# Optimization experiments

Hardware: AMD Instinct MI355X
Metric: run time of the kernel (lower is better)

## Reference

```python
import jax, jax.numpy as jnp
import numpy as np

B, S, D, H = 2, 2048, 768, 12
DK = D // H

def setup_inputs() -> dict:
    key = jax.random.key(0)
    ks = jax.random.split(key, 5)
    scale = 1.0 / np.sqrt(D)
    return {
        "X": jax.random.normal(ks[0], (B, S, D), dtype=jnp.float32),
        "Wq": jax.random.normal(ks[1], (D, D), dtype=jnp.float32) * scale,
        "Wk": jax.random.normal(ks[2], (D, D), dtype=jnp.float32) * scale,
        "Wv": jax.random.normal(ks[3], (D, D), dtype=jnp.float32) * scale,
        "Wo": jax.random.normal(ks[4], (D, D), dtype=jnp.float32) * scale,
    }

def reference(X, Wq, Wk, Wv, Wo):
    # torch Linear: y = x @ W.T  (no bias in this repo's Linear)
    Q = X @ Wq.T  # (B,S,D)
    K = X @ Wk.T
    V = X @ Wv.T
    def split_heads(t):
        return t.reshape(B, S, H, DK).transpose(0, 2, 1, 3)  # (B,H,S,DK)
    Qh, Kh, Vh = split_heads(Q), split_heads(K), split_heads(V)
    scores = jnp.einsum('bhqd,bhkd->bhqk', Qh, Kh) / jnp.sqrt(jnp.float32(DK))
    causal = jnp.tril(jnp.ones((S, S), dtype=bool))  # keep lower triangle
    scores = jnp.where(causal, scores, -jnp.inf)
    attn = jax.nn.softmax(scores, axis=-1)
    out_h = jnp.einsum('bhqk,bhkd->bhqd', attn, Vh)  # (B,H,S,DK)
    out = out_h.transpose(0, 2, 1, 3).reshape(B, S, D)
    return out @ Wo.T
```

## Files before the change

kernel.cpp:

```cpp
#include <hip/hip_runtime.h>
#include <stdint.h>

#define BB   2
#define SS   2048
#define DD   768
#define HH   12
#define MM   (BB*SS)
#define XSZ  (MM*DD)
#define WSZ  (DD*DD)

typedef __bf16 v8bf __attribute__((ext_vector_type(8)));
typedef float  v4f  __attribute__((ext_vector_type(4)));

__device__ inline v4f mfma16(v8bf a, v8bf b, v4f c) {
    return __builtin_amdgcn_mfma_f32_16x16x32_bf16(a, b, c, 0, 0, 0);
}

__device__ inline unsigned short f2bf(float f) {
    union { float f; uint32_t u; } v; v.f = f;
    return (unsigned short)((v.u + 0x7FFFu + ((v.u >> 16) & 1u)) >> 16);
}

__device__ inline uint4 cvt8(const float* __restrict__ p) {
    uint4 out;
    unsigned short* s = (unsigned short*)&out;
#pragma unroll
    for (int j = 0; j < 8; ++j) s[j] = f2bf(p[j]);
    return out;
}

__device__ __forceinline__ void gld_lds16(const unsigned short* g, unsigned short* l) {
    __builtin_amdgcn_global_load_lds(
        (const __attribute__((address_space(1))) void*)g,
        (__attribute__((address_space(3))) void*)l, 16, 0, 0);
}

__global__ __launch_bounds__(256) void cvt_w3(
    const float* __restrict__ Wq, const float* __restrict__ Wk,
    const float* __restrict__ Wv, unsigned short* __restrict__ dst)
{
    long i4 = ((long)blockIdx.x * 256 + threadIdx.x) * 4;
    int t = (int)(i4 / WSZ);
    long off = i4 - (long)t * WSZ;
    const float* s = (t == 0) ? Wq : (t == 1) ? Wk : Wv;
    float4 v = *(const float4*)(s + off);
    ushort4 o;
    o.x = f2bf(v.x); o.y = f2bf(v.y); o.z = f2bf(v.z); o.w = f2bf(v.w);
    *(ushort4*)(dst + (size_t)t * WSZ + off) = o;
}

template<int A_ASYNC, int W_ASYNC, int C_F32, int VT2>
__global__ __launch_bounds__(256) void gemm_64(
    const void* __restrict__ Ain,
    const void* __restrict__ W0, const void* __restrict__ W1,
    const void* __restrict__ W2,
    void* __restrict__ C0, void* __restrict__ C1, void* __restrict__ C2)
{
    const int K = DD, N = DD;
    const void* W = W0;
    void* C = C0;
    if (blockIdx.z == 1) { W = W1; C = C1; }
    else if (blockIdx.z == 2) { W = W2; C = C2; }

    __shared__ __align__(16) unsigned short As[64 * 32];
    __shared__ __align__(16) unsigned short Bs[64 * 32];

    const int tid  = threadIdx.x;
    const int wave = tid >> 6, lane = tid & 63;
    const int quad = lane >> 4, l16 = lane & 15;
    const int waveM = (wave >> 1) * 32, waveN = (wave & 1) * 32;
    const int m0 = blockIdx.y * 64, n0 = blockIdx.x * 64;

    const int rS = (tid >> 2), cS = (tid & 3) * 8;

    v4f acc[2][2] = {};

    for (int kt = 0; kt < K; kt += 32) {
        __syncthreads();
        if (A_ASYNC)
            gld_lds16((const unsigned short*)Ain + (size_t)(m0 + rS) * K + kt + cS,
                      &As[wave * 512]);
        else
            *(uint4*)(&As[tid * 8]) = cvt8((const float*)Ain + (size_t)(m0 + rS) * K + kt + cS);
        if (W_ASYNC)
            gld_lds16((const unsigned short*)W + (size_t)(n0 + rS) * K + kt + cS,
                      &Bs[wave * 512]);
        else
            *(uint4*)(&Bs[tid * 8]) = cvt8((const float*)W + (size_t)(n0 + rS) * K + kt + cS);
        __syncthreads();

        v8bf af[2], bf[2];
#pragma unroll
        for (int i = 0; i < 2; ++i) {
            af[i] = *(const v8bf*)(&As[(waveM + i * 16 + l16) * 32 + quad * 8]);
            bf[i] = *(const v8bf*)(&Bs[(waveN + i * 16 + l16) * 32 + quad * 8]);
        }
#pragma unroll
        for (int mi = 0; mi < 2; ++mi)
#pragma unroll
            for (int ni = 0; ni < 2; ++ni)
                acc[mi][ni] = mfma16(af[mi], bf[ni], acc[mi][ni]);
    }

#pragma unroll
    for (int mi = 0; mi < 2; ++mi)
#pragma unroll
        for (int ni = 0; ni < 2; ++ni)
#pragma unroll
            for (int r = 0; r < 4; ++r) {
                int row = m0 + waveM + mi * 16 + quad * 4 + r;
                int col = n0 + waveN + ni * 16 + l16;
                if (VT2 && blockIdx.z == 2) {
                    int b = row >> 11, s = row & 2047;
                    int h = col >> 6,  dk = col & 63;
                    ((unsigned short*)C)[(((size_t)(b * HH + h)) * 64 + dk) * SS + s] =
                        f2bf(acc[mi][ni][r]);
                } else if (C_F32) {
                    ((float*)C)[(size_t)row * N + col] = acc[mi][ni][r];
                } else {
                    ((unsigned short*)C)[(size_t)row * N + col] = f2bf(acc[mi][ni][r]);
                }
            }
}

__global__ __launch_bounds__(256, 3) void attn_ls(
    const unsigned short* Q,
    const unsigned short* __restrict__ Kg,
    const unsigned short* __restrict__ Vt,
    unsigned short* O)
{
    const int h = blockIdx.x, b = blockIdx.y;
    const int qs = (SS / 64 - 1 - (int)blockIdx.z) * 64;
    const int tid  = threadIdx.x;
    const int wave = tid >> 6, lane = tid & 63;
    const int quad = lane >> 4, l16 = lane & 15;
    const int qw = qs + wave * 16;
    const float scale = 0.125f;

    __shared__ __align__(16) unsigned short Ks[2][4096];
    __shared__ __align__(16) unsigned short Vs[2][4096];
    __shared__ __align__(16) unsigned short Ps[4][16 * 72];

    v8bf qf0, qf1;
    {
        const unsigned short* qp = &Q[((size_t)(b * SS + qw + l16)) * DD + h * 64];
        qf0 = *(const v8bf*)(qp + quad * 8);
        qf1 = *(const v8bf*)(qp + 32 + quad * 8);
    }

    const int NT = qs / 64 + 1;
    const char* kgb = (const char*)&Kg[(size_t)(b * SS) * DD + h * 64];
    const char* vgb = (const char*)&Vt[((size_t)(b * HH + h) * 64) * SS];

    const int rA = wave * 8 + (lane >> 3);
    const int oA = ((lane & 7) * 16) ^ ((rA & 7) << 4);
    const int swz = (l16 & 7) << 4;

    v4f oacc[4] = {};
    float l_run[4] = {0.f, 0.f, 0.f, 0.f};
    unsigned short* pw = &Ps[wave][0];

    gld_lds16((const unsigned short*)(kgb + (size_t)rA        * (DD * 2) + oA), &Ks[0][wave * 512]);
    gld_lds16((const unsigned short*)(kgb + (size_t)(rA + 32) * (DD * 2) + oA), &Ks[0][2048 + wave * 512]);
    gld_lds16((const unsigned short*)(vgb + (size_t)rA        * (SS * 2) + oA), &Vs[0][wave * 512]);
    gld_lds16((const unsigned short*)(vgb + (size_t)(rA + 32) * (SS * 2) + oA), &Vs[0][2048 + wave * 512]);
    __syncthreads();

    for (int kt = 0; kt < NT; ++kt) {
        const int cur = kt & 1;
        const int kb  = kt * 64;

        if (kt + 1 < NT) {
            const size_t kb2 = (size_t)(kb + 64);
            gld_lds16((const unsigned short*)(kgb + (kb2 + rA)      * (DD * 2) + oA), &Ks[cur ^ 1][wave * 512]);
            gld_lds16((const unsigned short*)(kgb + (kb2 + rA + 32) * (DD * 2) + oA), &Ks[cur ^ 1][2048 + wave * 512]);
            gld_lds16((const unsigned short*)(vgb + (size_t)rA        * (SS * 2) + kb2 * 2 + oA), &Vs[cur ^ 1][wave * 512]);
            gld_lds16((const unsigned short*)(vgb + (size_t)(rA + 32) * (SS * 2) + kb2 * 2 + oA), &Vs[cur ^ 1][2048 + wave * 512]);
        }

        const char* ksb = (const char*)&Ks[cur][0];
        const char* vsb = (const char*)&Vs[cur][0];

        v8bf kf0[4], kf1[4];
#pragma unroll
        for (int nk = 0; nk < 4; ++nk) {
            const char* krow = ksb + (size_t)(nk * 16 + l16) * 128;
            kf0[nk] = *(const v8bf*)(krow + ((quad * 16) ^ swz));
            kf1[nk] = *(const v8bf*)(krow + ((64 + quad * 16) ^ swz));
        }

        v4f sacc[4] = {};
#pragma unroll
        for (int nk = 0; nk < 4; ++nk) {
            sacc[nk] = mfma16(qf0, kf0[nk], sacc[nk]);
            sacc[nk] = mfma16(qf1, kf1[nk], sacc[nk]);
        }

        const bool diag = (kt == NT - 1);
        float pv[4][4];
#pragma unroll
        for (int nk = 0; nk < 4; ++nk)
#pragma unroll
            for (int r = 0; r < 4; ++r) {
                float p = __expf(sacc[nk][r] * scale);
                if (diag) {
                    int key  = kb + nk * 16 + l16;
                    int qrow = qw + quad * 4 + r;
                    if (key > qrow) p = 0.0f;
                }
                pv[nk][r] = p;
                l_run[r] += p;
            }

        v8bf vf[2][4];
#pragma unroll
        for (int kc = 0; kc < 2; ++kc)
#pragma unroll
            for (int dt = 0; dt < 4; ++dt) {
                const char* vr = vsb + (size_t)(dt * 16 + l16) * 128;
                vf[kc][dt] = *(const v8bf*)(vr + ((kc * 64 + quad * 16) ^ swz));
            }

#pragma unroll
        for (int nk = 0; nk < 4; ++nk)
#pragma unroll
            for (int r = 0; r < 4; ++r)
                pw[(quad * 4 + r) * 72 + nk * 16 + l16] = f2bf(pv[nk][r]);
        __asm__ volatile("" ::: "memory");

        v8bf pa0 = *(const v8bf*)(&pw[l16 * 72 + quad * 8]);
        v8bf pa1 = *(const v8bf*)(&pw[l16 * 72 + 32 + quad * 8]);
#pragma unroll
        for (int dt = 0; dt < 4; ++dt) oacc[dt] = mfma16(pa0, vf[0][dt], oacc[dt]);
#pragma unroll
        for (int dt = 0; dt < 4; ++dt) oacc[dt] = mfma16(pa1, vf[1][dt], oacc[dt]);

        __syncthreads();
    }

    for (int off = 1; off < 16; off <<= 1)
#pragma unroll
        for (int r = 0; r < 4; ++r)
            l_run[r] += __shfl_xor(l_run[r], off, 64);

    float inv[4];
#pragma unroll
    for (int r = 0; r < 4; ++r) inv[r] = 1.0f / l_run[r];

    unsigned short* ob = &O[((size_t)(b * SS + qw + quad * 4)) * DD + h * 64 + l16];
#pragma unroll
    for (int r = 0; r < 4; ++r)
#pragma unroll
        for (int dt = 0; dt < 4; ++dt)
            ob[(size_t)r * DD + dt * 16] = f2bf(oacc[dt][r] * inv[r]);
}

extern "C" void kernel_launch(void* const* d_in, const int* in_sizes, int n_in,
                              void* d_out, int out_size, void* d_ws, size_t ws_size,
                              hipStream_t stream)
{
    const float* X  = (const float*)d_in[0];
    const float* Wq = (const float*)d_in[1];
    const float* Wk = (const float*)d_in[2];
    const float* Wv = (const float*)d_in[3];
    const float* Wo = (const float*)d_in[4];
    float* Out = (float*)d_out;

    unsigned short* Qb  = (unsigned short*)d_ws;
    unsigned short* Kb  = Qb + XSZ;
    unsigned short* Vtb = (unsigned short*)d_out;
    unsigned short* Wqb = Vtb + XSZ;
    unsigned short* Wkb = Wqb + WSZ;
    unsigned short* Wvb = Wkb + WSZ;

    dim3 blk(256);
    cvt_w3<<<1728, blk, 0, stream>>>(Wq, Wk, Wv, Wqb);

    dim3 g1(DD / 64, MM / 64, 3);
    gemm_64<0, 1, 0, 1><<<g1, blk, 0, stream>>>(X, Wqb, Wkb, Wvb, Qb, Kb, Vtb);

    dim3 g2(HH, BB, SS / 64);
    attn_ls<<<g2, blk, 0, stream>>>(Qb, Kb, Vtb, Qb);

    dim3 g3(DD / 64, MM / 64, 1);
    gemm_64<1, 0, 1, 0><<<g3, blk, 0, stream>>>(Qb, Wo, Wo, Wo, Out, Out, Out);
}
```

Before: 183.3 us.

## Fuse QKV projections into one kernel sharing converted X tiles

Replaces the three-way z-indexed QKV GEMM with one kernel that converts each X tile to bf16 once and multiplies it against Wq, Wk and Wv tiles held together in LDS, using a 64-deep K step, XOR-swizzled shared layouts and a grouped block ordering. It also pre-converts Wo to bf16 into the free K buffer so the output GEMM can load weights asynchronously. The aim is to cut repeated X loads and fp32 conversions and to shrink weight traffic. In exchange it raises LDS use and accumulator register pressure, which may lower occupancy, and it adds an extra conversion launch.

```diff
diff --git a/kernel.cpp b/kernel.cpp
--- a/kernel.cpp
+++ b/kernel.cpp
@@ -49,18 +49,118 @@
     *(ushort4*)(dst + (size_t)t * WSZ + off) = o;
 }
 
-template<int A_ASYNC, int W_ASYNC, int C_F32, int VT2>
+__global__ __launch_bounds__(256) void cvt_wo(
+    const float* __restrict__ Wo, unsigned short* __restrict__ dst)
+{
+    long i4 = ((long)blockIdx.x * 256 + threadIdx.x) * 4;
+    float4 v = *(const float4*)(Wo + i4);
+    ushort4 o;
+    o.x = f2bf(v.x); o.y = f2bf(v.y); o.z = f2bf(v.z); o.w = f2bf(v.w);
+    *(ushort4*)(dst + i4) = o;
+}
+
+__global__ __launch_bounds__(256) void gemm_qkv(
+    const float* __restrict__ X,
+    const unsigned short* __restrict__ Wq,
+    const unsigned short* __restrict__ Wk,
+    const unsigned short* __restrict__ Wv,
+    unsigned short* __restrict__ Qo,
+    unsigned short* __restrict__ Ko,
+    unsigned short* __restrict__ Vo)
+{
+    __shared__ __align__(16) unsigned short As[64 * 64];
+    __shared__ __align__(16) unsigned short Bs[3][64 * 64];
+
+    const int flat = (int)(blockIdx.y * gridDim.x + blockIdx.x);
+    const int sw   = (flat & 7) * 96 + (flat >> 3);
+    const int m0   = (sw / 12) * 64;
+    const int n0   = (sw % 12) * 64;
+
+    const int tid  = threadIdx.x;
+    const int wave = tid >> 6, lane = tid & 63;
+    const int quad = lane >> 4, l16 = lane & 15;
+    const int waveM = (wave >> 1) * 32, waveN = (wave & 1) * 32;
+
+    const int rA  = tid >> 2;
+    const int cA  = (tid & 3) * 16;
+    const int rxA = (rA & 7) << 4;
+
+    const int rB  = wave * 8 + (lane >> 3);
+    const int cB  = ((lane & 7) ^ (lane >> 3)) * 8;
+
+    const int swz = (l16 & 7) << 4;
+
+    v4f acc[3][2][2] = {};
+
+    const float* ap0 = X + (size_t)(m0 + rA) * DD + cA;
+    const unsigned short* w0 = Wq + (size_t)(n0 + rB) * DD + cB;
+    const unsigned short* w1 = Wk + (size_t)(n0 + rB) * DD + cB;
+    const unsigned short* w2 = Wv + (size_t)(n0 + rB) * DD + cB;
+
+    for (int kt = 0; kt < DD; kt += 64) {
+        __syncthreads();
+        *(uint4*)((char*)As + rA * 128 + ((cA * 2)      ^ rxA)) = cvt8(ap0 + kt);
+        *(uint4*)((char*)As + rA * 128 + ((cA * 2 + 16) ^ rxA)) = cvt8(ap0 + kt + 8);
+        gld_lds16(w0 + kt,           &Bs[0][wave * 512]);
+        gld_lds16(w0 + kt + 32 * DD, &Bs[0][2048 + wave * 512]);
+        gld_lds16(w1 + kt,           &Bs[1][wave * 512]);
+        gld_lds16(w1 + kt + 32 * DD, &Bs[1][2048 + wave * 512]);
+        gld_lds16(w2 + kt,           &Bs[2][wave * 512]);
+        gld_lds16(w2 + kt + 32 * DD, &Bs[2][2048 + wave * 512]);
+        __syncthreads();
+
+        v8bf af[2][2];
+#pragma unroll
+        for (int mi = 0; mi < 2; ++mi) {
+            const char* arow = (const char*)As + (size_t)(waveM + mi * 16 + l16) * 128;
+#pragma unroll
+            for (int kf = 0; kf < 2; ++kf)
+                af[mi][kf] = *(const v8bf*)(arow + ((kf * 64 + quad * 16) ^ swz));
+        }
+#pragma unroll
+        for (int z = 0; z < 3; ++z) {
+            v8bf bfr[2][2];
+#pragma unroll
+            for (int ni = 0; ni < 2; ++ni) {
+                const char* brow = (const char*)&Bs[z][0] + (size_t)(waveN + ni * 16 + l16) * 128;
+#pragma unroll
+                for (int kf = 0; kf < 2; ++kf)
+                    bfr[ni][kf] = *(const v8bf*)(brow + ((kf * 64 + quad * 16) ^ swz));
+            }
+#pragma unroll
+            for (int mi = 0; mi < 2; ++mi)
+#pragma unroll
+                for (int ni = 0; ni < 2; ++ni) {
+                    acc[z][mi][ni] = mfma16(af[mi][0], bfr[ni][0], acc[z][mi][ni]);
+                    acc[z][mi][ni] = mfma16(af[mi][1], bfr[ni][1], acc[z][mi][ni]);
+                }
+        }
+    }
+
+#pragma unroll
+    for (int mi = 0; mi < 2; ++mi)
+#pragma unroll
+        for (int ni = 0; ni < 2; ++ni)
+#pragma unroll
+            for (int r = 0; r < 4; ++r) {
+                const int row = m0 + waveM + mi * 16 + quad * 4 + r;
+                const int col = n0 + waveN + ni * 16 + l16;
+                Qo[(size_t)row * DD + col] = f2bf(acc[0][mi][ni][r]);
+                Ko[(size_t)row * DD + col] = f2bf(acc[1][mi][ni][r]);
+                const int b = row >> 11, s = row & 2047;
+                const int h = col >> 6,  dk = col & 63;
+                Vo[(((size_t)(b * HH + h)) * 64 + dk) * SS + s] = f2bf(acc[2][mi][ni][r]);
+            }
+}
+
+template<int A_ASYNC, int W_ASYNC, int C_F32>
 __global__ __launch_bounds__(256) void gemm_64(
-    const void* __restrict__ Ain,
-    const void* __restrict__ W0, const void* __restrict__ W1,
-    const void* __restrict__ W2,
-    void* __restrict__ C0, void* __restrict__ C1, void* __restrict__ C2)
+    const void* __restrict__ Ain, const void* __restrict__ W0,
+    void* __restrict__ C0)
 {
     const int K = DD, N = DD;
     const void* W = W0;
     void* C = C0;
-    if (blockIdx.z == 1) { W = W1; C = C1; }
-    else if (blockIdx.z == 2) { W = W2; C = C2; }
 
     __shared__ __align__(16) unsigned short As[64 * 32];
     __shared__ __align__(16) unsigned short Bs[64 * 32];
@@ -110,12 +210,7 @@
             for (int r = 0; r < 4; ++r) {
                 int row = m0 + waveM + mi * 16 + quad * 4 + r;
                 int col = n0 + waveN + ni * 16 + l16;
-                if (VT2 && blockIdx.z == 2) {
-                    int b = row >> 11, s = row & 2047;
-                    int h = col >> 6,  dk = col & 63;
-                    ((unsigned short*)C)[(((size_t)(b * HH + h)) * 64 + dk) * SS + s] =
-                        f2bf(acc[mi][ni][r]);
-                } else if (C_F32) {
+                if (C_F32) {
                     ((float*)C)[(size_t)row * N + col] = acc[mi][ni][r];
                 } else {
                     ((unsigned short*)C)[(size_t)row * N + col] = f2bf(acc[mi][ni][r]);
@@ -276,12 +371,14 @@
     dim3 blk(256);
     cvt_w3<<<1728, blk, 0, stream>>>(Wq, Wk, Wv, Wqb);
 
-    dim3 g1(DD / 64, MM / 64, 3);
-    gemm_64<0, 1, 0, 1><<<g1, blk, 0, stream>>>(X, Wqb, Wkb, Wvb, Qb, Kb, Vtb);
+    dim3 g1(DD / 64, MM / 64);
+    gemm_qkv<<<g1, blk, 0, stream>>>(X, Wqb, Wkb, Wvb, Qb, Kb, Vtb);
 
     dim3 g2(HH, BB, SS / 64);
     attn_ls<<<g2, blk, 0, stream>>>(Qb, Kb, Vtb, Qb);
 
-    dim3 g3(DD / 64, MM / 64, 1);
-    gemm_64<1, 0, 1, 0><<<g3, blk, 0, stream>>>(Qb, Wo, Wo, Wo, Out, Out, Out);
-}
+    cvt_wo<<<576, blk, 0, stream>>>(Wo, Kb);
+
+    dim3 g3(DD / 64, MM / 64);
+    gemm_64<1, 1, 1><<<g3, blk, 0, stream>>>(Qb, Kb, Out);
+}
```

Result: faster. 158.8 us (-13.4%).
